# Performance work log

Hardware: AMD Instinct MI355X
Metric: run time of the kernel (lower is better)

## Reference

```python
import jax, jax.numpy as jnp
import numpy as np
import math

B, L = 4, 4096
D_MODEL = 1024
D_INNER = 1024          # expand=1
D_STATE = 1             # required by rearrange 'b d 1 l' in ssm()
D_CONV = 2
DT_RANK = 64            # ceil(1024/16)
EPS = 1e-5


def setup_inputs() -> dict:
    key = jax.random.key(0)
    ks = jax.random.split(key, 8)
    dt_min, dt_max, dt_floor = 1e-3, 1e-1, 1e-4
    # dt_proj bias init: inverse-softplus of log-uniform dt (faithful to dt_init)
    dt = jnp.exp(jax.random.uniform(ks[5], (D_INNER,)) * (math.log(dt_max) - math.log(dt_min)) + math.log(dt_min))
    dt = jnp.clip(dt, dt_floor, None)
    inv_dt = dt + jnp.log(-jnp.expm1(-dt))
    std = DT_RANK ** -0.5
    return {
        "x": jax.random.normal(ks[0], (B, L, D_MODEL), dtype=jnp.float32),
        "w_in": jax.random.normal(ks[1], (2 * D_INNER, D_MODEL), dtype=jnp.float32) * 0.02,
        "conv_w": jax.random.normal(ks[2], (D_INNER, 1, D_CONV), dtype=jnp.float32) * 0.5,
        "conv_b": jnp.zeros((D_INNER,), dtype=jnp.float32),
        "x_proj_weight": jax.random.normal(ks[3], (DT_RANK + 2 * D_STATE, D_INNER), dtype=jnp.float32) * 0.02,
        "dt_projs_weight": jax.random.uniform(ks[4], (D_INNER, DT_RANK), minval=-std, maxval=std, dtype=jnp.float32),
        "dt_projs_bias": inv_dt,
        "A_logs": jnp.tile(jnp.log(jnp.arange(1, D_STATE + 1, dtype=jnp.float32))[None, :], (D_INNER, 1)),
        "Ds": jnp.ones((D_INNER,), dtype=jnp.float32),
        "ln_w": jnp.ones((D_INNER,), dtype=jnp.float32),
        "ln_b": jnp.zeros((D_INNER,), dtype=jnp.float32),
        "w_out": jax.random.normal(ks[6], (D_MODEL, D_INNER), dtype=jnp.float32) * 0.02,
    }


def _selective_scan(u, delta, A, Bs):
    # u, delta: (B, D, L); A: (D, N); Bs: (B, N, L) -> hidden states h: (B, D, N, L)
    dA = jnp.exp(jnp.einsum('bdl,dn->bdnl', delta, A))            # (B,D,N,L)
    dBu = jnp.einsum('bdl,bnl,bdl->bdnl', delta, Bs, u)           # delta * B * u
    dA_t = jnp.moveaxis(dA, -1, 0)                                # (L,B,D,N)
    dBu_t = jnp.moveaxis(dBu, -1, 0)

    def step(h, inp):
        a_t, bu_t = inp
        h = a_t * h + bu_t
        return h, h

    h0 = jnp.zeros(dA.shape[:-1], dtype=u.dtype)
    _, hs = jax.lax.scan(step, h0, (dA_t, dBu_t))                 # (L,B,D,N)
    return jnp.moveaxis(hs, 0, -1)                                # (B,D,N,L)


def reference(x, w_in, conv_w, conv_b, x_proj_weight, dt_projs_weight,
              dt_projs_bias, A_logs, Ds, ln_w, ln_b, w_out):
    Bsz, Lsz, _ = x.shape
    # in_proj (bias=False), chunk into x and gate z
    xz = x @ w_in.T                                               # (B,L,2*D)
    xc, z = xz[..., :D_INNER], xz[..., D_INNER:]
    xc = jnp.transpose(xc, (0, 2, 1))                             # (B,D,L)
    # depthwise causal conv1d, padding=d_conv-1, truncated to L
    xc = jax.lax.conv_general_dilated(
        xc, conv_w, window_strides=(1,), padding=[(D_CONV - 1, D_CONV - 1)],
        feature_group_count=D_INNER,
        dimension_numbers=('NCH', 'OIH', 'NCH'))[..., :Lsz]
    xc = xc + conv_b[None, :, None]
    xc = jax.nn.silu(xc)
    # ssm()
    x_dbl = jnp.einsum('rd,bdl->brl', x_proj_weight, xc)          # (B,R+2N,L)
    dts = x_dbl[:, :DT_RANK]
    Bs = x_dbl[:, DT_RANK:DT_RANK + D_STATE]                      # (B,N,L)
    Cs = x_dbl[:, DT_RANK + D_STATE:]                             # (B,N,L)
    dts = jnp.einsum('dr,brl->bdl', dt_projs_weight, dts)         # (B,D,L)
    A = -jnp.exp(A_logs)                                          # (D,N)
    delta = jax.nn.softplus(dts + dt_projs_bias[None, :, None])   # delta_softplus=True
    h = _selective_scan(xc, delta, A, Bs)                         # (B,D,N,L)
    h = h.reshape(Bsz, D_INNER * D_STATE, Lsz)                    # 'b d 1 l -> b (d 1) l' (N==1)
    y = h * Cs + xc * Ds[:, None]                                 # (B,D,L)
    # out_norm (LayerNorm over d_inner), gate, out_proj
    y = jnp.transpose(y, (0, 2, 1))                               # (B,L,D)
    mu = jnp.mean(y, axis=-1, keepdims=True)
    var = jnp.mean(jnp.square(y - mu), axis=-1, keepdims=True)
    y = (y - mu) * jax.lax.rsqrt(var + EPS) * ln_w + ln_b
    y = y * jax.nn.silu(z)
    return y @ w_out.T                                            # (B,L,d_model)
```

## Files before the change

### kernel.cpp

```cpp
#include <hip/hip_runtime.h>
#include <hip/hip_bf16.h>
#include <cstdint>
#include <cstddef>

typedef short short8 __attribute__((ext_vector_type(8)));
typedef short short4v __attribute__((ext_vector_type(4)));
typedef float floatx4 __attribute__((ext_vector_type(4)));

constexpr int Bz = 4;
constexpr int Lz = 4096;
constexpr int Dm = 1024;
constexpr int Di = 1024;
constexpr int Mrows = Bz * Lz;
constexpr int CH  = 128;
constexpr int NCH = Lz / CH;
constexpr int XPJ_KS = 4;

__device__ __forceinline__ void load16(const void* g, void* l) {
  __builtin_amdgcn_global_load_lds((__attribute__((address_space(1))) void*)g,
                                   (__attribute__((address_space(3))) void*)l,
                                   16, 0, 0);
}

__device__ __forceinline__ float bf2f(const __hip_bfloat16 v) { return __bfloat162float(v); }
__device__ __forceinline__ short f2bfs(float v) {
  __hip_bfloat16 h = __float2bfloat16(v);
  return *(short*)&h;
}

__global__ __launch_bounds__(256) void cvt_bf16(const float* __restrict__ in,
                                                __hip_bfloat16* __restrict__ out, int n4)
{
  const int i = blockIdx.x * 256 + threadIdx.x;
  if (i >= n4) return;
  const float4 v = ((const float4*)in)[i];
  short4v s;
  s[0] = f2bfs(v.x); s[1] = f2bfs(v.y); s[2] = f2bfs(v.z); s[3] = f2bfs(v.w);
  ((short4v*)out)[i] = s;
}

__global__ __launch_bounds__(256) void cvt_weights(
    const float* __restrict__ w_in, const float* __restrict__ w_out,
    const float* __restrict__ xpw, const float* __restrict__ dtw,
    __hip_bfloat16* __restrict__ w_in_bf, __hip_bfloat16* __restrict__ w_out_bf,
    __hip_bfloat16* __restrict__ xpw_bf, __hip_bfloat16* __restrict__ dtw_bf)
{
  const int i = blockIdx.x * 256 + threadIdx.x;
  const float* src; __hip_bfloat16* dst; int j;
  if (i < 524288)      { src = w_in;  dst = w_in_bf;  j = i; }
  else if (i < 786432) { src = w_out; dst = w_out_bf; j = i - 524288; }
  else if (i < 803328) { src = xpw;   dst = xpw_bf;   j = i - 786432; }
  else if (i < 819712) { src = dtw;   dst = dtw_bf;   j = i - 803328; }
  else return;
  const float4 v = ((const float4*)src)[j];
  short4v s;
  s[0] = f2bfs(v.x); s[1] = f2bfs(v.y); s[2] = f2bfs(v.z); s[3] = f2bfs(v.w);
  ((short4v*)dst)[j] = s;
}

template <int EPI>
__global__ __launch_bounds__(256) void gemm128(
    const __hip_bfloat16* __restrict__ A,
    const __hip_bfloat16* __restrict__ W,
    int K, int N,
    __hip_bfloat16* __restrict__ outb0,
    __hip_bfloat16* __restrict__ outb1,
    float* __restrict__ outf,
    const float* __restrict__ biasf)
{
  constexpr int BK = 32;
  constexpr int GY = 16;
  __shared__ short sA[128 * BK];
  __shared__ short sB[128 * BK];
  const int tid  = threadIdx.x;
  const int wid  = tid >> 6;
  const int lane = tid & 63;

  const int gx  = gridDim.x;
  const int id  = blockIdx.y * gx + blockIdx.x;
  const int seg = gx * GY;
  const int bx  = (id % seg) / GY;
  const int by  = (id / seg) * GY + (id % GY);

  const int m0 = by * 128;
  const int n0 = bx * 128;
  const int wm = (wid & 1) * 64;
  const int wn = (wid >> 1) * 64;

  floatx4 acc[4][4];
#pragma unroll
  for (int i = 0; i < 4; i++)
#pragma unroll
    for (int j = 0; j < 4; j++) acc[i][j] = (floatx4){0.f, 0.f, 0.f, 0.f};

  const short* Ag = (const short*)A + (size_t)(m0 + (tid >> 2)) * K + (tid & 3) * 8;
  const short* Bg = (const short*)W + (size_t)(n0 + (tid >> 2)) * K + (tid & 3) * 8;
  short* sAd = &sA[tid * 8];
  short* sBd = &sB[tid * 8];
  const size_t rstep = (size_t)64 * K;
  const int fr = lane & 15, fq = lane >> 4;

  for (int kb = 0; kb < K; kb += BK) {
    load16(Ag, sAd);
    load16(Ag + rstep, sAd + 2048);
    load16(Bg, sBd);
    load16(Bg + rstep, sBd + 2048);
    Ag += BK; Bg += BK;
    __syncthreads();

    short8 av[4], bv[4];
#pragma unroll
    for (int mt = 0; mt < 4; mt++) av[mt] = *(const short8*)&sA[(wm + mt * 16 + fr) * BK + fq * 8];
#pragma unroll
    for (int nt = 0; nt < 4; nt++) bv[nt] = *(const short8*)&sB[(wn + nt * 16 + fr) * BK + fq * 8];
#pragma unroll
    for (int mt = 0; mt < 4; mt++)
#pragma unroll
      for (int nt = 0; nt < 4; nt++)
        acc[mt][nt] = __builtin_amdgcn_mfma_f32_16x16x32_bf16(av[mt], bv[nt], acc[mt][nt], 0, 0, 0);
    __syncthreads();
  }

#pragma unroll
  for (int mt = 0; mt < 4; mt++) {
#pragma unroll
    for (int nt = 0; nt < 4; nt++) {
#pragma unroll
      for (int r = 0; r < 4; r++) {
        const int gm = m0 + wm + mt * 16 + fq * 4 + r;
        const int gn = n0 + wn + nt * 16 + fr;
        float v = acc[mt][nt][r];
        if constexpr (EPI == 0) {
          if (gn < 1024) outb0[(size_t)gm * 1024 + gn] = __float2bfloat16(v);
          else           outb1[(size_t)gm * 1024 + (gn - 1024)] = __float2bfloat16(v);
        } else if constexpr (EPI == 1) {
          v += biasf[gn];
          v = (v > 15.f) ? v : __logf(1.f + __expf(v));
          outb0[(size_t)gm * N + gn] = __float2bfloat16(v);
        } else {
          outf[(size_t)gm * N + gn] = v;
        }
      }
    }
  }
}

template <int EPI>
__device__ __forceinline__ void cluster_mfma(int MQ, floatx4 (&acc)[8][4],
                                             const short8 (&av)[8][2],
                                             const short8 (&bv)[4][2])
{
  __builtin_amdgcn_s_setprio(1);
#pragma unroll
  for (int j = 0; j < 2; j++)
#pragma unroll
    for (int nf = 0; nf < 4; nf++)
#pragma unroll
      for (int ks = 0; ks < 2; ks++)
        acc[2 * MQ + j][nf] = __builtin_amdgcn_mfma_f32_16x16x32_bf16(
            av[2 * MQ + j][ks], bv[nf][ks], acc[2 * MQ + j][nf], 0, 0, 0);
  __builtin_amdgcn_s_setprio(0);
}

template <int EPI>
__global__ __launch_bounds__(512, 2) void gemm256(
    const __hip_bfloat16* __restrict__ A,
    const __hip_bfloat16* __restrict__ W,
    int K, int N,
    __hip_bfloat16* __restrict__ outb0,
    __hip_bfloat16* __restrict__ outb1,
    float* __restrict__ outf)
{
  __shared__ alignas(16) char lds[131072];
  const int tid  = threadIdx.x;
  const int wid  = tid >> 6;
  const int lane = tid & 63;
  const int wm = wid >> 2;
  const int wn = wid & 3;
  const int fr = lane & 15, fq = lane >> 4;
  const int m0 = blockIdx.y * 256;
  const int n0 = blockIdx.x * 256;
  const size_t K2 = (size_t)K * 2;

  int rowo[2], colo[2];
#pragma unroll
  for (int i = 0; i < 2; i++) {
    const int p = i * 8192 + tid * 16;
    const int s = p >> 10;
    const int r = (p >> 6) & 15;
    rowo[i] = (s >> 1) * 16 + r;
    colo[i] = (s & 1) * 64 + ((p & 63) ^ (((r >> 3) & 1) << 5));
  }
  const char* Ab = (const char*)A + (size_t)m0 * K2;
  const char* Bb = (const char*)W + (size_t)n0 * K2;
  char* lbase = (char*)lds;

#define STAGE_A(c, h, kt) do {                                                          \
    load16(Ab + (size_t)((h) * 128 + rowo[0]) * K2 + (size_t)(kt) * 128 + colo[0],      \
           lbase + (c) * 32768 + (h) * 16384 + tid * 16);                               \
    load16(Ab + (size_t)((h) * 128 + rowo[1]) * K2 + (size_t)(kt) * 128 + colo[1],      \
           lbase + (c) * 32768 + (h) * 16384 + 8192 + tid * 16);                        \
  } while (0)
#define STAGE_B(c, h, kt) do {                                                          \
    load16(Bb + (size_t)((h) * 128 + rowo[0]) * K2 + (size_t)(kt) * 128 + colo[0],      \
           lbase + 65536 + (c) * 32768 + (h) * 16384 + tid * 16);                       \
    load16(Bb + (size_t)((h) * 128 + rowo[1]) * K2 + (size_t)(kt) * 128 + colo[1],      \
           lbase + 65536 + (c) * 32768 + (h) * 16384 + 8192 + tid * 16);                \
  } while (0)

  const int foff = (fr * 64 + fq * 16) ^ (((fr >> 3) & 1) << 5);

  floatx4 acc[8][4];
#pragma unroll
  for (int i = 0; i < 8; i++)
#pragma unroll
    for (int j = 0; j < 4; j++) acc[i][j] = (floatx4){0.f, 0.f, 0.f, 0.f};

  STAGE_A(0, 0, 0); STAGE_A(0, 1, 0); STAGE_B(0, 0, 0); STAGE_B(0, 1, 0);
  STAGE_B(1, 0, 1); STAGE_B(1, 1, 1); STAGE_A(1, 0, 1);
  asm volatile("s_waitcnt vmcnt(6)\n\ts_barrier" ::: "memory");

  const int NT = K >> 6;
  short8 av[8][2], bv[4][2];
#pragma unroll 2
  for (int t = 0; t < NT; ++t) {
    const int cur = t & 1, nxt = cur ^ 1;
    const char* la = lbase + cur * 32768 + wm * 16384 + foff;
    const char* lb = lbase + 65536 + cur * 32768 + (wn >> 1) * 16384 + (wn & 1) * 8192 + foff;

#pragma unroll
    for (int nf = 0; nf < 4; nf++)
#pragma unroll
      for (int ks = 0; ks < 2; ks++)
        bv[nf][ks] = *(const short8*)(lb + (nf * 2 + ks) * 1024);
#pragma unroll
    for (int mf = 0; mf < 2; mf++)
#pragma unroll
      for (int ks = 0; ks < 2; ks++)
        av[mf][ks] = *(const short8*)(la + (mf * 2 + ks) * 1024);
    if (t + 1 < NT) STAGE_A(nxt, 1, t + 1);
    asm volatile("s_barrier" ::: "memory");
    asm volatile("s_waitcnt lgkmcnt(0)" ::: "memory");
    cluster_mfma<EPI>(0, acc, av, bv);
    asm volatile("s_barrier" ::: "memory");

#pragma unroll
    for (int mf = 2; mf < 4; mf++)
#pragma unroll
      for (int ks = 0; ks < 2; ks++)
        av[mf][ks] = *(const short8*)(la + (mf * 2 + ks) * 1024);
    if (t + 2 < NT) STAGE_B(cur, 0, t + 2);
    asm volatile("s_barrier" ::: "memory");
    asm volatile("s_waitcnt lgkmcnt(0)" ::: "memory");
    cluster_mfma<EPI>(1, acc, av, bv);
    asm volatile("s_barrier" ::: "memory");

#pragma unroll
    for (int mf = 4; mf < 8; mf++)
#pragma unroll
      for (int ks = 0; ks < 2; ks++)
        av[mf][ks] = *(const short8*)(la + (mf * 2 + ks) * 1024);
    if (t + 2 < NT) STAGE_B(cur, 1, t + 2);
    asm volatile("s_barrier" ::: "memory");
    asm volatile("s_waitcnt lgkmcnt(0)" ::: "memory");
    cluster_mfma<EPI>(2, acc, av, bv);
    asm volatile("s_barrier" ::: "memory");

    if (t + 2 < NT) STAGE_A(cur, 0, t + 2);
    asm volatile("s_barrier" ::: "memory");
    cluster_mfma<EPI>(3, acc, av, bv);
    if (t < NT - 2) {
      asm volatile("s_waitcnt vmcnt(6)\n\ts_barrier" ::: "memory");
    } else if (t == NT - 2) {
      asm volatile("s_waitcnt vmcnt(0)\n\ts_barrier" ::: "memory");
    }
  }
#undef STAGE_A
#undef STAGE_B

#pragma unroll
  for (int mf = 0; mf < 8; mf++) {
#pragma unroll
    for (int nf = 0; nf < 4; nf++) {
#pragma unroll
      for (int r = 0; r < 4; r++) {
        const int gm = m0 + wm * 128 + mf * 16 + fq * 4 + r;
        const int gn = n0 + wn * 64 + nf * 16 + fr;
        const float v = acc[mf][nf][r];
        if constexpr (EPI == 0) {
          if (gn < 1024) outb0[(size_t)gm * 1024 + gn] = __float2bfloat16(v);
          else           outb1[(size_t)gm * 1024 + (gn - 1024)] = __float2bfloat16(v);
        } else {
          outf[(size_t)gm * N + gn] = v;
        }
      }
    }
  }
}

__global__ __launch_bounds__(256) void gemm_xproj(
    const __hip_bfloat16* __restrict__ A,
    const __hip_bfloat16* __restrict__ W,
    float* __restrict__ part)
{
  constexpr int K = 1024, BK = 32, KC = K / XPJ_KS;
  __shared__ short sA[128 * BK];
  __shared__ short sB[80 * BK];
  const int tid = threadIdx.x;
  const int wid = tid >> 6, lane = tid & 63;
  const int kc = blockIdx.x;
  const int m0 = blockIdx.y * 128;

  floatx4 acc[2][5];
#pragma unroll
  for (int i = 0; i < 2; i++)
#pragma unroll
    for (int j = 0; j < 5; j++) acc[i][j] = (floatx4){0.f, 0.f, 0.f, 0.f};

  const short* Ag = (const short*)A + (size_t)(m0 + (tid >> 2)) * K + kc * KC + (tid & 3) * 8;
  const int brow2 = 64 + (tid >> 2);
  const int brow2c = brow2 > 65 ? 65 : brow2;
  const short* Bg  = (const short*)W + (size_t)(tid >> 2) * K + kc * KC + (tid & 3) * 8;
  const short* Bg2 = (const short*)W + (size_t)brow2c * K + kc * KC + (tid & 3) * 8;
  const size_t rstep = (size_t)64 * K;
  const int fr = lane & 15, fq = lane >> 4;

  for (int kb = 0; kb < KC; kb += BK) {
    load16(Ag, &sA[tid * 8]);
    load16(Ag + rstep, &sA[2048 + tid * 8]);
    load16(Bg, &sB[tid * 8]);
    if (tid < 64) load16(Bg2, &sB[2048 + tid * 8]);
    Ag += BK; Bg += BK; Bg2 += BK;
    __syncthreads();

    short8 av[2], bv[5];
#pragma unroll
    for (int mt = 0; mt < 2; mt++) av[mt] = *(const short8*)&sA[(wid * 32 + mt * 16 + fr) * BK + fq * 8];
#pragma unroll
    for (int nt = 0; nt < 5; nt++) bv[nt] = *(const short8*)&sB[(nt * 16 + fr) * BK + fq * 8];
#pragma unroll
    for (int mt = 0; mt < 2; mt++)
#pragma unroll
      for (int nt = 0; nt < 5; nt++)
        acc[mt][nt] = __builtin_amdgcn_mfma_f32_16x16x32_bf16(av[mt], bv[nt], acc[mt][nt], 0, 0, 0);
    __syncthreads();
  }

  float* pp = part + (size_t)kc * Mrows * 66;
#pragma unroll
  for (int mt = 0; mt < 2; mt++) {
#pragma unroll
    for (int nt = 0; nt < 5; nt++) {
#pragma unroll
      for (int r = 0; r < 4; r++) {
        const int gm = m0 + wid * 32 + mt * 16 + fq * 4 + r;
        const int gn = nt * 16 + fr;
        if (gn < 66) pp[(size_t)gm * 66 + gn] = acc[mt][nt][r];
      }
    }
  }
}

__global__ __launch_bounds__(256) void xproj_reduce(
    const float* __restrict__ part,
    __hip_bfloat16* __restrict__ dts,
    float* __restrict__ Bs, float* __restrict__ Cs)
{
  const int i = blockIdx.x * 256 + threadIdx.x;
  if (i >= Mrows * 66) return;
  const int gm = i / 66, gn = i - gm * 66;
  float s = part[i] + part[i + (size_t)Mrows * 66]
          + part[i + (size_t)2 * Mrows * 66] + part[i + (size_t)3 * Mrows * 66];
  if (gn < 64)       dts[(size_t)gm * 64 + gn] = __float2bfloat16(s);
  else if (gn == 64) Bs[gm] = s;
  else               Cs[gm] = s;
}

__global__ __launch_bounds__(256) void conv_silu(
    const __hip_bfloat16* __restrict__ xc, const float* __restrict__ cw,
    const float* __restrict__ cb, __hip_bfloat16* __restrict__ u)
{
  const size_t idx = (size_t)blockIdx.x * 256 + threadIdx.x;
  const int d = (int)(idx & (Di - 1));
  const int l = (int)((idx >> 10) & (Lz - 1));
  const float w0 = cw[2 * d], w1 = cw[2 * d + 1];
  const float prev = (l > 0) ? bf2f(xc[idx - Di]) : 0.f;
  const float v = prev * w0 + bf2f(xc[idx]) * w1 + cb[d];
  const float s = v / (1.f + __expf(-v));
  u[idx] = __float2bfloat16(s);
}

__global__ __launch_bounds__(256) void scan_p1(
    const __hip_bfloat16* __restrict__ delta, const __hip_bfloat16* __restrict__ u,
    const float* __restrict__ Bsv, const float* __restrict__ A_logs,
    float* __restrict__ carryP, float* __restrict__ carryS)
{
  const int d = blockIdx.x * 256 + threadIdx.x;
  const int c = blockIdx.y, b = blockIdx.z;
  const float Ac = -__expf(A_logs[d]);
  size_t base = ((size_t)(b * Lz + c * CH)) * Di + d;
  const float* Bp = Bsv + (size_t)b * Lz + c * CH;
  float P = 1.f, h = 0.f;
#pragma unroll 4
  for (int j = 0; j < CH; j++) {
    const float dl = bf2f(delta[base + (size_t)j * Di]);
    const float uu = bf2f(u[base + (size_t)j * Di]);
    const float a  = __expf(dl * Ac);
    h = a * h + dl * Bp[j] * uu;
    P *= a;
  }
  const int ci = (b * NCH + c) * Di + d;
  carryP[ci] = P;
  carryS[ci] = h;
}

__global__ __launch_bounds__(256) void scan_p2(
    const float* __restrict__ carryP, const float* __restrict__ carryS,
    float* __restrict__ hin)
{
  const int t = blockIdx.x * 256 + threadIdx.x;
  const int b = t >> 10, d = t & (Di - 1);
  float h = 0.f;
  for (int c = 0; c < NCH; c++) {
    const int ci = (b * NCH + c) * Di + d;
    hin[ci] = h;
    h = carryP[ci] * h + carryS[ci];
  }
}

__global__ __launch_bounds__(256) void scan_p3(
    const __hip_bfloat16* __restrict__ delta, __hip_bfloat16* __restrict__ uy,
    const float* __restrict__ Bsv, const float* __restrict__ Csv,
    const float* __restrict__ A_logs, const float* __restrict__ Ds,
    const float* __restrict__ hin)
{
  const int d = blockIdx.x * 256 + threadIdx.x;
  const int c = blockIdx.y, b = blockIdx.z;
  const float Ac = -__expf(A_logs[d]);
  const float Dd = Ds[d];
  size_t base = ((size_t)(b * Lz + c * CH)) * Di + d;
  const float* Bp = Bsv + (size_t)b * Lz + c * CH;
  const float* Cp = Csv + (size_t)b * Lz + c * CH;
  float h = hin[(b * NCH + c) * Di + d];
#pragma unroll 4
  for (int j = 0; j < CH; j++) {
    const size_t ix = base + (size_t)j * Di;
    const float dl = bf2f(delta[ix]);
    const float uu = bf2f(uy[ix]);
    const float a  = __expf(dl * Ac);
    h = a * h + dl * Bp[j] * uu;
    uy[ix] = __float2bfloat16(h * Cp[j] + uu * Dd);
  }
}

__global__ __launch_bounds__(256) void ln_gate(
    const __hip_bfloat16* __restrict__ y, const __hip_bfloat16* __restrict__ z,
    const float* __restrict__ lnw, const float* __restrict__ lnb,
    __hip_bfloat16* __restrict__ yg)
{
  const int row = blockIdx.x;
  const int tid = threadIdx.x;
  const int wid = tid >> 6, lane = tid & 63;
  const short4v yv = *(const short4v*)((const short*)y + (size_t)row * Di + tid * 4);
  float v[4];
#pragma unroll
  for (int i = 0; i < 4; i++) {
    __hip_bfloat16 t;
    *(short*)&t = yv[i];
    v[i] = bf2f(t);
  }
  float s1 = v[0] + v[1] + v[2] + v[3];
  float s2 = v[0] * v[0] + v[1] * v[1] + v[2] * v[2] + v[3] * v[3];
#pragma unroll
  for (int o = 32; o > 0; o >>= 1) {
    s1 += __shfl_down(s1, o, 64);
    s2 += __shfl_down(s2, o, 64);
  }
  __shared__ float r1[4], r2[4];
  if (lane == 0) { r1[wid] = s1; r2[wid] = s2; }
  __syncthreads();
  const float t1 = r1[0] + r1[1] + r1[2] + r1[3];
  const float t2 = r2[0] + r2[1] + r2[2] + r2[3];
  const float mu = t1 * (1.f / Di);
  const float var = t2 * (1.f / Di) - mu * mu;
  const float rstd = rsqrtf(var + 1e-5f);

  const float4 wv = ((const float4*)lnw)[tid];
  const float4 bv = ((const float4*)lnb)[tid];
  const float wa[4] = {wv.x, wv.y, wv.z, wv.w};
  const float ba[4] = {bv.x, bv.y, bv.z, bv.w};
  const __hip_bfloat16* zr = z + (size_t)row * Di + tid * 4;
  __hip_bfloat16* outp = yg + (size_t)row * Di + tid * 4;
#pragma unroll
  for (int i = 0; i < 4; i++) {
    const float zv = bf2f(zr[i]);
    const float g = zv / (1.f + __expf(-zv));
    outp[i] = __float2bfloat16(((v[i] - mu) * rstd * wa[i] + ba[i]) * g);
  }
}

__global__ __launch_bounds__(256) void fill_diag(float* __restrict__ out, int n, float val)
{
  const int i = blockIdx.x * 256 + threadIdx.x;
  if (i < n) out[i] = val;
}

extern "C" void kernel_launch(void* const* d_in, const int* in_sizes, int n_in,
                              void* d_out, int out_size, void* d_ws, size_t ws_size,
                              hipStream_t stream)
{
  const float* x      = (const float*)d_in[0];
  const float* w_in   = (const float*)d_in[1];
  const float* conv_w = (const float*)d_in[2];
  const float* conv_b = (const float*)d_in[3];
  const float* xpw    = (const float*)d_in[4];
  const float* dtw    = (const float*)d_in[5];
  const float* dtb    = (const float*)d_in[6];
  const float* A_logs = (const float*)d_in[7];
  const float* Ds     = (const float*)d_in[8];
  const float* lnw    = (const float*)d_in[9];
  const float* lnb    = (const float*)d_in[10];
  const float* w_out  = (const float*)d_in[11];
  float* outF = (float*)d_out;

  const size_t BF16BIG  = (size_t)Mrows * Di * sizeof(__hip_bfloat16);
  const size_t NEED_RUN = 69603328;

  if (ws_size < NEED_RUN) {
    fill_diag<<<(out_size + 255) / 256, 256, 0, stream>>>(
        outF, out_size, (float)(ws_size >> 10));
    return;
  }

  uint8_t* ws = (uint8_t*)d_ws;
  size_t off = 0;
  auto alloc = [&](size_t bytes) { void* p = ws + off; off += (bytes + 255) & ~(size_t)255; return p; };

  __hip_bfloat16* slotA    = (__hip_bfloat16*)alloc(BF16BIG);
  __hip_bfloat16* slotC    = (__hip_bfloat16*)alloc(BF16BIG);
  __hip_bfloat16* w_out_bf = (__hip_bfloat16*)alloc((size_t)Dm * Di * 2);
  __hip_bfloat16* xpw_bf   = (__hip_bfloat16*)alloc((size_t)66 * Di * 2);
  __hip_bfloat16* dtw_bf   = (__hip_bfloat16*)alloc((size_t)Di * 64 * 2);
  float* Bsv = (float*)alloc((size_t)Mrows * sizeof(float));
  float* Csv = (float*)alloc((size_t)Mrows * sizeof(float));

  __hip_bfloat16* zbuf    = (__hip_bfloat16*)d_out;
  __hip_bfloat16* w_in_bf = (__hip_bfloat16*)((uint8_t*)d_out + 33554432);
  uint8_t* dts_region     = (uint8_t*)d_out + 37748736;
  float* xpj_part         = (float*)((uint8_t*)d_out + 41943040);
  __hip_bfloat16* dts = (__hip_bfloat16*)dts_region;
  float* carryP = (float*)dts_region;
  float* carryS = carryP + (size_t)Bz * NCH * Di;
  float* hin    = carryS + (size_t)Bz * NCH * Di;

  __hip_bfloat16* xbf   = slotC;
  __hip_bfloat16* xcbuf = slotA;
  __hip_bfloat16* ubuf  = slotC;
  __hip_bfloat16* delta = slotA;
  __hip_bfloat16* yg    = slotA;

  cvt_bf16<<<(Mrows * Di / 4 + 255) / 256, 256, 0, stream>>>(x, xbf, Mrows * Di / 4);
  cvt_weights<<<(819712 + 255) / 256, 256, 0, stream>>>(
      w_in, w_out, xpw, dtw, w_in_bf, w_out_bf, xpw_bf, dtw_bf);

  gemm256<0><<<dim3(2 * Di / 256, Mrows / 256), 512, 0, stream>>>(
      xbf, w_in_bf, Dm, 2 * Di, xcbuf, zbuf, nullptr);
  conv_silu<<<(Mrows * Di) / 256, 256, 0, stream>>>(xcbuf, conv_w, conv_b, ubuf);
  gemm_xproj<<<dim3(XPJ_KS, Mrows / 128), 256, 0, stream>>>(ubuf, xpw_bf, xpj_part);
  xproj_reduce<<<(Mrows * 66 + 255) / 256, 256, 0, stream>>>(xpj_part, dts, Bsv, Csv);
  gemm128<1><<<dim3(Di / 128, Mrows / 128), 256, 0, stream>>>(
      dts, dtw_bf, 64, Di, delta, nullptr, nullptr, dtb);
  scan_p1<<<dim3(Di / 256, NCH, Bz), 256, 0, stream>>>(delta, ubuf, Bsv, A_logs, carryP, carryS);
  scan_p2<<<(Bz * Di) / 256, 256, 0, stream>>>(carryP, carryS, hin);
  scan_p3<<<dim3(Di / 256, NCH, Bz), 256, 0, stream>>>(delta, ubuf, Bsv, Csv, A_logs, Ds, hin);
  ln_gate<<<Mrows, 256, 0, stream>>>(ubuf, zbuf, lnw, lnb, yg);
  gemm256<1><<<dim3(Dm / 256, Mrows / 256), 512, 0, stream>>>(
      yg, w_out_bf, Di, Dm, nullptr, nullptr, outF);
}
```

Before: 380.4 us.

## Swizzle GEMM workgroup order and replace asm barriers with builtin sched barriers

Remaps the linear workgroup index so consecutive blocks are spread across groups of eight (an XCD-aware swizzle), meant to improve L2 reuse of A and W tiles on the multi-die GPU. It also replaces inline-asm barriers, which carried memory clobbers, with __builtin_amdgcn_s_barrier plus sched_barrier fences around the waitcnts. That gives the compiler scheduling freedom without the clobbers, but dropping them risks reordering LDS reads unless the sched_barrier holds the order. The swizzle assumes the block count is divisible by 8.

New measurement: 365.7 us. -3.9%, faster.

```diff
diff --git a/kernel.cpp b/kernel.cpp
--- a/kernel.cpp
+++ b/kernel.cpp
@@ -145,6 +145,11 @@
   }
 }
 
+__device__ __forceinline__ void wait_lgkm0() {
+  asm volatile("s_waitcnt lgkmcnt(0)");
+  __builtin_amdgcn_sched_barrier(0);
+}
+
 template <int EPI>
 __device__ __forceinline__ void cluster_mfma(int MQ, floatx4 (&acc)[8][4],
                                              const short8 (&av)[8][2],
@@ -178,8 +183,15 @@
   const int wm = wid >> 2;
   const int wn = wid & 3;
   const int fr = lane & 15, fq = lane >> 4;
-  const int m0 = blockIdx.y * 256;
-  const int n0 = blockIdx.x * 256;
+
+  const int gx   = gridDim.x;
+  const int nwg  = gx * gridDim.y;
+  const int orig = blockIdx.y * gx + blockIdx.x;
+  const int swz  = (orig & 7) * (nwg >> 3) + (orig >> 3);
+  const int bx   = swz % gx;
+  const int by   = swz / gx;
+  const int m0 = by * 256;
+  const int n0 = bx * 256;
   const size_t K2 = (size_t)K * 2;
 
   int rowo[2], colo[2];
@@ -218,7 +230,9 @@
 
   STAGE_A(0, 0, 0); STAGE_A(0, 1, 0); STAGE_B(0, 0, 0); STAGE_B(0, 1, 0);
   STAGE_B(1, 0, 1); STAGE_B(1, 1, 1); STAGE_A(1, 0, 1);
-  asm volatile("s_waitcnt vmcnt(6)\n\ts_barrier" ::: "memory");
+  asm volatile("s_waitcnt vmcnt(6)");
+  __builtin_amdgcn_sched_barrier(0);
+  __builtin_amdgcn_s_barrier();
 
   const int NT = K >> 6;
   short8 av[8][2], bv[4][2];
@@ -239,10 +253,10 @@
       for (int ks = 0; ks < 2; ks++)
         av[mf][ks] = *(const short8*)(la + (mf * 2 + ks) * 1024);
     if (t + 1 < NT) STAGE_A(nxt, 1, t + 1);
-    asm volatile("s_barrier" ::: "memory");
-    asm volatile("s_waitcnt lgkmcnt(0)" ::: "memory");
+    __builtin_amdgcn_s_barrier();
+    wait_lgkm0();
     cluster_mfma<EPI>(0, acc, av, bv);
-    asm volatile("s_barrier" ::: "memory");
+    __builtin_amdgcn_s_barrier();
 
 #pragma unroll
     for (int mf = 2; mf < 4; mf++)
@@ -250,10 +264,10 @@
       for (int ks = 0; ks < 2; ks++)
         av[mf][ks] = *(const short8*)(la + (mf * 2 + ks) * 1024);
     if (t + 2 < NT) STAGE_B(cur, 0, t + 2);
-    asm volatile("s_barrier" ::: "memory");
-    asm volatile("s_waitcnt lgkmcnt(0)" ::: "memory");
+    __builtin_amdgcn_s_barrier();
+    wait_lgkm0();
     cluster_mfma<EPI>(1, acc, av, bv);
-    asm volatile("s_barrier" ::: "memory");
+    __builtin_amdgcn_s_barrier();
 
 #pragma unroll
     for (int mf = 4; mf < 8; mf++)
@@ -261,18 +275,22 @@
       for (int ks = 0; ks < 2; ks++)
         av[mf][ks] = *(const short8*)(la + (mf * 2 + ks) * 1024);
     if (t + 2 < NT) STAGE_B(cur, 1, t + 2);
-    asm volatile("s_barrier" ::: "memory");
-    asm volatile("s_waitcnt lgkmcnt(0)" ::: "memory");
+    __builtin_amdgcn_s_barrier();
+    wait_lgkm0();
     cluster_mfma<EPI>(2, acc, av, bv);
-    asm volatile("s_barrier" ::: "memory");
+    __builtin_amdgcn_s_barrier();
 
     if (t + 2 < NT) STAGE_A(cur, 0, t + 2);
-    asm volatile("s_barrier" ::: "memory");
+    __builtin_amdgcn_s_barrier();
     cluster_mfma<EPI>(3, acc, av, bv);
     if (t < NT - 2) {
-      asm volatile("s_waitcnt vmcnt(6)\n\ts_barrier" ::: "memory");
+      asm volatile("s_waitcnt vmcnt(6)");
+      __builtin_amdgcn_sched_barrier(0);
+      __builtin_amdgcn_s_barrier();
     } else if (t == NT - 2) {
-      asm volatile("s_waitcnt vmcnt(0)\n\ts_barrier" ::: "memory");
+      asm volatile("s_waitcnt vmcnt(0)");
+      __builtin_amdgcn_sched_barrier(0);
+      __builtin_amdgcn_s_barrier();
     }
   }
 #undef STAGE_A
```
